# Optimization experiments

Measured on AMD Instinct MI355X. Metric: run time of the kernel, lower is better.

## Reference

```python
import jax, jax.numpy as jnp
import numpy as np

B, T, D = 8, 8192, 768
H, HD = 12, 64            # heads, head_dim
Q_STRIDE = 4              # flattened 2x2 q pooling
WINDOW = 64               # flattened mask-unit size after pooling
SCALE = HD ** -0.5


def setup_inputs() -> dict:
    key = jax.random.key(0)
    ks = jax.random.split(key, 5)
    return {
        "embeddings": jax.random.normal(ks[0], (B, T, D), jnp.float32),
        "qkv_w": jax.random.normal(ks[1], (3 * D, D), jnp.float32) * 0.02,
        "qkv_b": jax.random.normal(ks[2], (3 * D,), jnp.float32) * 0.02,
        "proj_w": jax.random.normal(ks[3], (D, D), jnp.float32) * 0.02,
        "proj_b": jax.random.normal(ks[4], (D,), jnp.float32) * 0.02,
    }


def reference(embeddings, qkv_w, qkv_b, proj_w, proj_b):
    b, t, _ = embeddings.shape
    nw = t // (Q_STRIDE * WINDOW)          # number of mask-unit windows
    seq = t // nw                           # tokens per window (pre q-pool)
    # qkv: [b, t, 3D] -> [b, seq, nw, 3, H, HD] (windows are interleaved along tokens)
    qkv = (embeddings @ qkv_w.T + qkv_b).reshape(b, seq, nw, 3, H, HD)
    qkv = jnp.transpose(qkv, (3, 0, 4, 2, 1, 5))  # [3, b, H, nw, seq, HD]
    q, k, v = qkv[0], qkv[1], qkv[2]
    # q max-pool over stride groups (interleaved split of seq)
    q = q.reshape(b, H, nw, Q_STRIDE, seq // Q_STRIDE, HD).max(axis=3)
    attn = jax.nn.softmax(
        jnp.einsum("bhwqd,bhwkd->bhwqk", q * SCALE, k), axis=-1
    )  # [b, H, nw, q_len, seq]
    out = jnp.einsum("bhwqk,bhwkd->bhwqd", attn, v)  # [b, H, nw, q_len, HD]
    out = jnp.transpose(out, (0, 3, 2, 1, 4)).reshape(b, -1, H * HD)
    out = out @ proj_w.T + proj_b
    return out, attn
```

## Files before the change

kernel.cpp:

```cpp
#include <hip/hip_runtime.h>
#include <hip/hip_bf16.h>


typedef float  f32x4  __attribute__((ext_vector_type(4)));
typedef __bf16 bf16x8 __attribute__((ext_vector_type(8)));

__device__ __forceinline__ unsigned short f2bf(float f) {
  unsigned int u = __float_as_uint(f);
  u += 0x7fffu + ((u >> 16) & 1u);
  return (unsigned short)(u >> 16);
}
__device__ __forceinline__ float bf2f(unsigned short b) {
  return __uint_as_float(((unsigned int)b) << 16);
}

#define GLOAD_LDS16(gptr, lptr) __builtin_amdgcn_global_load_lds( \
    (const __attribute__((address_space(1))) void*)(gptr),        \
    (__attribute__((address_space(3))) void*)(lptr), 16, 0, 0)

__global__ void cvt_bf16(const float* __restrict__ src,
                         unsigned short* __restrict__ dst, int n4) {
  int i = blockIdx.x * blockDim.x + threadIdx.x;
  const int stride = gridDim.x * blockDim.x;
  for (; i < n4; i += stride) {
    const float4 v = ((const float4*)src)[i];
    ushort4 o;
    o.x = f2bf(v.x); o.y = f2bf(v.y); o.z = f2bf(v.z); o.w = f2bf(v.w);
    ((ushort4*)dst)[i] = o;
  }
}

__global__ void cvt_w2(const float* __restrict__ s1, unsigned short* __restrict__ d1,
                       int n1_4,
                       const float* __restrict__ s2, unsigned short* __restrict__ d2,
                       int n2_4) {
  int i = blockIdx.x * blockDim.x + threadIdx.x;
  const int stride = gridDim.x * blockDim.x;
  const int tot = n1_4 + n2_4;
  for (; i < tot; i += stride) {
    const float4 v = (i < n1_4) ? ((const float4*)s1)[i]
                                : ((const float4*)s2)[i - n1_4];
    ushort4 o;
    o.x = f2bf(v.x); o.y = f2bf(v.y); o.z = f2bf(v.z); o.w = f2bf(v.w);
    if (i < n1_4) ((ushort4*)d1)[i] = o;
    else          ((ushort4*)d2)[i - n1_4] = o;
  }
}

template <int OUT_BF16>
__global__ __launch_bounds__(512, 2) void gemm256p(
    const unsigned short* __restrict__ A, const unsigned short* __restrict__ B,
    const float* __restrict__ bias, void* __restrict__ Cout,
    int M, int N, int K) {
  extern __shared__ char lds[];

  const int tid  = threadIdx.x;
  const int lane = tid & 63;
  const int wid  = tid >> 6;
  const int g16  = (lane >> 4) & 3;
  const int l15  = lane & 15;
  const int wm   = wid >> 2;
  const int wn   = wid & 3;

  const size_t bm = (size_t)blockIdx.x << 8;
  const int NT = K >> 6;
  const int NB = N >> 8;
  const int TT = NB * NT;

  const int srow = tid >> 2;
  const int csel = (((tid & 3) ^ ((tid >> 3) & 3)) << 3);
  const int ldst = wid * 1024;
  const unsigned short* pA0 = A + (bm + srow) * (size_t)K + csel;
  const unsigned short* pA1 = pA0 + (size_t)128 * K;
  const unsigned short* pB0 = B + (size_t)srow * K + csel;
  const unsigned short* pB1 = pB0 + (size_t)128 * K;

#define STAGE_A(koff, regbase)                                          \
  do {                                                                  \
    GLOAD_LDS16(pA0 + (koff), lds + (regbase) + ldst);                  \
    GLOAD_LDS16(pA1 + (koff), lds + (regbase) + 8192 + ldst);           \
  } while (0)
#define STAGE_B(boff, regbase)                                          \
  do {                                                                  \
    GLOAD_LDS16(pB0 + (boff), lds + (regbase) + ldst);                  \
    GLOAD_LDS16(pB1 + (boff), lds + (regbase) + 8192 + ldst);           \
  } while (0)

  const int s16  = ((g16 ^ ((l15 >> 1) & 3)) << 4);
  const int offA = (wm * 128 + l15) * 64 + s16;
  const int offB = (wn * 64 + l15) * 64 + s16;

  f32x4 acc[8][4];
  const f32x4 zero4 = {0.f, 0.f, 0.f, 0.f};
#pragma unroll
  for (int i = 0; i < 8; ++i)
#pragma unroll
    for (int j = 0; j < 4; ++j) acc[i][j] = zero4;

#define READ_A(par, kk, rh)                                              \
  { const char* rb = lds + (par) * 32768 + (kk) * 16384 + offA + (rh) * 4096; \
    af[0] = *(const bf16x8*)(rb);                                        \
    af[1] = *(const bf16x8*)(rb + 1024);                                 \
    af[2] = *(const bf16x8*)(rb + 2048);                                 \
    af[3] = *(const bf16x8*)(rb + 3072); }
#define READ_B(par, kk)                                                  \
  { const char* rb = lds + 65536 + (par) * 32768 + (kk) * 16384 + offB;  \
    bfv[0] = *(const bf16x8*)(rb);                                       \
    bfv[1] = *(const bf16x8*)(rb + 1024);                                \
    bfv[2] = *(const bf16x8*)(rb + 2048);                                \
    bfv[3] = *(const bf16x8*)(rb + 3072); }
#define MFMA16(rh)                                                       \
  _Pragma("unroll") for (int q = 0; q < 4; ++q)                          \
  _Pragma("unroll") for (int c = 0; c < 4; ++c)                          \
    acc[(rh) * 4 + q][c] = __builtin_amdgcn_mfma_f32_16x16x32_bf16(      \
        af[q], bfv[c], acc[(rh) * 4 + q][c], 0, 0, 0);
#define BAR() __builtin_amdgcn_s_barrier()
#define VMCNT8() asm volatile("s_waitcnt vmcnt(8)" ::: "memory")

  int    kk  = 0;
  int    bnC = 0;
  int    k1  = 64;
  int    k2  = 128;
  size_t rB1 = 0;
  size_t rB2 = 0;

  STAGE_A(0, 0);
  STAGE_B(0, 65536);
  STAGE_A(32, 16384);
  STAGE_B(32, 65536 + 16384);
  STAGE_A(64, 32768);
  STAGE_B(64, 65536 + 32768);
  VMCNT8();
  BAR();

  for (int s = 0; s < TT; ++s) {
    const int par  = s & 1;
    const int parn = par ^ 1;
    bf16x8 af[4], bfv[4];

    READ_A(par, 0, 0); READ_B(par, 0);
    STAGE_A(k1 + 32, parn * 32768 + 16384);
    BAR();
    __builtin_amdgcn_s_setprio(1); MFMA16(0); __builtin_amdgcn_s_setprio(0);
    BAR();

    READ_A(par, 0, 1);
    STAGE_B(rB1 + k1 + 32, 65536 + parn * 32768 + 16384);
    VMCNT8();
    BAR();
    __builtin_amdgcn_s_setprio(1); MFMA16(1); __builtin_amdgcn_s_setprio(0);
    BAR();

    READ_A(par, 1, 0); READ_B(par, 1);
    STAGE_A(k2, par * 32768);
    BAR();
    __builtin_amdgcn_s_setprio(1); MFMA16(0); __builtin_amdgcn_s_setprio(0);
    BAR();

    READ_A(par, 1, 1);
    STAGE_B(rB2 + k2, 65536 + par * 32768);
    VMCNT8();
    BAR();
    __builtin_amdgcn_s_setprio(1); MFMA16(1); __builtin_amdgcn_s_setprio(0);
    BAR();

    if (kk == NT - 1) {
#pragma unroll
      for (int ai = 0; ai < 8; ++ai) {
        const size_t row0 =
            bm + wm * 128 + (ai >> 2) * 64 + (ai & 3) * 16 + g16 * 4;
#pragma unroll
        for (int c = 0; c < 4; ++c) {
          const int col = bnC + wn * 64 + c * 16 + l15;
          const float bv = bias[col];
#pragma unroll
          for (int r = 0; r < 4; ++r) {
            const float v = acc[ai][c][r] + bv;
            const size_t idx = (row0 + r) * (size_t)N + col;
            if (OUT_BF16) ((unsigned short*)Cout)[idx] = f2bf(v);
            else          ((float*)Cout)[idx] = v;
          }
          acc[ai][c] = zero4;
        }
      }
      bnC += 256;
      kk = 0;
    } else {
      ++kk;
    }

    k1 = k2; rB1 = rB2;
    if (s + 3 < TT) {
      k2 += 64;
      if (k2 == K) { k2 = 0; rB2 += (size_t)256 * K; }
    }
  }
#undef STAGE_A
#undef STAGE_B
#undef READ_A
#undef READ_B
#undef MFMA16
#undef BAR
#undef VMCNT8
}

template <int OUT_BF16>
__global__ __launch_bounds__(512, 2) void gemm256t(
    const unsigned short* __restrict__ A, const unsigned short* __restrict__ B,
    const float* __restrict__ bias, void* __restrict__ Cout,
    int M, int N, int K) {
  extern __shared__ char lds[];

  const int tid  = threadIdx.x;
  const int lane = tid & 63;
  const int wid  = tid >> 6;
  const int g16  = (lane >> 4) & 3;
  const int l15  = lane & 15;
  const int wm   = wid >> 2;
  const int wn   = wid & 3;

  const int nbn = N >> 8;
  const int wg  = (blockIdx.x & 7) * ((int)gridDim.x >> 3) + (blockIdx.x >> 3);
  const size_t bm = (size_t)(wg / nbn) << 8;
  const size_t bn = (size_t)(wg % nbn) << 8;

  const int NT = K >> 6;

  const int srow = tid >> 2;
  const int csel = (((tid & 3) ^ ((tid >> 3) & 3)) << 3);
  const int ldst = wid * 1024;
  const unsigned short* pA0 = A + (bm + srow) * (size_t)K + csel;
  const unsigned short* pA1 = pA0 + (size_t)128 * K;
  const unsigned short* pB0 = B + (bn + srow) * (size_t)K + csel;
  const unsigned short* pB1 = pB0 + (size_t)128 * K;

#define STAGE(p0, p1, kcol, regbase)                                   \
  do {                                                                 \
    GLOAD_LDS16((p0) + (kcol), lds + (regbase) + ldst);                \
    GLOAD_LDS16((p1) + (kcol), lds + (regbase) + 8192 + ldst);         \
  } while (0)

  const int s16  = ((g16 ^ ((l15 >> 1) & 3)) << 4);
  const int offA = (wm * 128 + l15) * 64 + s16;
  const int offB = (wn * 64 + l15) * 64 + s16;

  f32x4 acc[8][4];
  const f32x4 zero4 = {0.f, 0.f, 0.f, 0.f};
#pragma unroll
  for (int i = 0; i < 8; ++i)
#pragma unroll
    for (int j = 0; j < 4; ++j) acc[i][j] = zero4;

#define READ_A(par, kk, rh)                                              \
  { const char* rb = lds + (par) * 32768 + (kk) * 16384 + offA + (rh) * 4096; \
    af[0] = *(const bf16x8*)(rb);                                        \
    af[1] = *(const bf16x8*)(rb + 1024);                                 \
    af[2] = *(const bf16x8*)(rb + 2048);                                 \
    af[3] = *(const bf16x8*)(rb + 3072); }
#define READ_B(par, kk)                                                  \
  { const char* rb = lds + 65536 + (par) * 32768 + (kk) * 16384 + offB;  \
    bfv[0] = *(const bf16x8*)(rb);                                       \
    bfv[1] = *(const bf16x8*)(rb + 1024);                                \
    bfv[2] = *(const bf16x8*)(rb + 2048);                                \
    bfv[3] = *(const bf16x8*)(rb + 3072); }
#define MFMA16(rh)                                                       \
  _Pragma("unroll") for (int q = 0; q < 4; ++q)                          \
  _Pragma("unroll") for (int c = 0; c < 4; ++c)                          \
    acc[(rh) * 4 + q][c] = __builtin_amdgcn_mfma_f32_16x16x32_bf16(      \
        af[q], bfv[c], acc[(rh) * 4 + q][c], 0, 0, 0);
#define BAR() __builtin_amdgcn_s_barrier()
#define VMCNT8() asm volatile("s_waitcnt vmcnt(8)" ::: "memory")

  STAGE(pA0, pA1, 0, 0);
  STAGE(pB0, pB1, 0, 65536);
  STAGE(pA0, pA1, 32, 16384);
  STAGE(pB0, pB1, 32, 65536 + 16384);
  {
    const int k1 = (NT > 1 ? 64 : 0);
    STAGE(pA0, pA1, k1, 32768);
    STAGE(pB0, pB1, k1, 65536 + 32768);
  }
  VMCNT8();
  BAR();

  for (int t = 0; t < NT; ++t) {
    const int par  = t & 1;
    const int parn = par ^ 1;
    const int kc1  = (t + 1 < NT ? t + 1 : NT - 1) * 64;
    const int kc2  = (t + 2 < NT ? t + 2 : NT - 1) * 64;
    bf16x8 af[4], bfv[4];

    READ_A(par, 0, 0); READ_B(par, 0);
    STAGE(pA0, pA1, kc1 + 32, parn * 32768 + 16384);
    BAR();
    __builtin_amdgcn_s_setprio(1); MFMA16(0); __builtin_amdgcn_s_setprio(0);
    BAR();

    READ_A(par, 0, 1);
    STAGE(pB0, pB1, kc1 + 32, 65536 + parn * 32768 + 16384);
    VMCNT8();
    BAR();
    __builtin_amdgcn_s_setprio(1); MFMA16(1); __builtin_amdgcn_s_setprio(0);
    BAR();

    READ_A(par, 1, 0); READ_B(par, 1);
    STAGE(pA0, pA1, kc2, par * 32768);
    BAR();
    __builtin_amdgcn_s_setprio(1); MFMA16(0); __builtin_amdgcn_s_setprio(0);
    BAR();

    READ_A(par, 1, 1);
    STAGE(pB0, pB1, kc2, 65536 + par * 32768);
    VMCNT8();
    BAR();
    __builtin_amdgcn_s_setprio(1); MFMA16(1); __builtin_amdgcn_s_setprio(0);
    BAR();
  }

#pragma unroll
  for (int ai = 0; ai < 8; ++ai) {
    const size_t row0 = bm + wm * 128 + (ai >> 2) * 64 + (ai & 3) * 16 + g16 * 4;
#pragma unroll
    for (int c = 0; c < 4; ++c) {
      const size_t col = bn + wn * 64 + c * 16 + l15;
      const float bv = bias[col];
#pragma unroll
      for (int r = 0; r < 4; ++r) {
        const float v = acc[ai][c][r] + bv;
        const size_t idx = (row0 + r) * N + col;
        if (OUT_BF16) ((unsigned short*)Cout)[idx] = f2bf(v);
        else          ((float*)Cout)[idx] = v;
      }
    }
  }
#undef STAGE
#undef READ_A
#undef READ_B
#undef MFMA16
#undef BAR
#undef VMCNT8
}

__global__ __launch_bounds__(256) void attn_kernel(
    const unsigned short* __restrict__ qkv,
    float* __restrict__ attn_out,
    unsigned short* __restrict__ Xws) {
  __shared__ unsigned short smem[32768];
  char* KP = (char*)smem;
  char* VT = (char*)(smem + 16384);

  const int tid  = threadIdx.x;
  const int lane = tid & 63;
  const int wid  = tid >> 6;
  const int g16  = lane >> 4;
  const int l15  = lane & 15;

  const int bid = blockIdx.x;
  const int w = bid & 31;
  const int h = (bid >> 5) % 12;
  const int b = bid / 384;

  const int s0 = tid >> 3;
  const int part = tid & 7;

#pragma unroll
  for (int p = 0; p < 8; ++p) {
    const int s = s0 + p * 32;
    const size_t gbase =
        ((size_t)b * 8192 + (size_t)s * 32 + w) * 2304 + h * 64 + part * 8;
    int4 kv = *(const int4*)(qkv + gbase + 768);
    *(int4*)(KP + ((s * 128 + part * 16) ^ ((s & 7) << 4))) = kv;
  }

#pragma unroll
  for (int p = 0; p < 2; ++p) {
    const int s = s0 * 4 + p * 128;
    const size_t gb0 =
        ((size_t)b * 8192 + (size_t)s * 32 + w) * 2304 + 1536 + h * 64 + part * 8;
    int4 x0 = *(const int4*)(qkv + gb0);
    int4 x1 = *(const int4*)(qkv + gb0 + 73728);
    int4 x2 = *(const int4*)(qkv + gb0 + 147456);
    int4 x3 = *(const int4*)(qkv + gb0 + 221184);
    const unsigned int* u0 = (const unsigned int*)&x0;
    const unsigned int* u1 = (const unsigned int*)&x1;
    const unsigned int* u2 = (const unsigned int*)&x2;
    const unsigned int* u3 = (const unsigned int*)&x3;
#pragma unroll
    for (int k = 0; k < 4; ++k) {
      const unsigned int lo01 = (u0[k] & 0xffffu) | (u1[k] << 16);
      const unsigned int lo23 = (u2[k] & 0xffffu) | (u3[k] << 16);
      const unsigned int hi01 = (u0[k] >> 16) | (u1[k] & 0xffff0000u);
      const unsigned int hi23 = (u2[k] >> 16) | (u3[k] & 0xffff0000u);
      const int dlo = part * 8 + 2 * k;
      const int dhi = dlo + 1;
      uint2 vlo; vlo.x = lo01; vlo.y = lo23;
      uint2 vhi; vhi.x = hi01; vhi.y = hi23;
      *(uint2*)(VT + ((dlo * 512 + s * 2) ^ ((dlo & 7) << 4))) = vlo;
      *(uint2*)(VT + ((dhi * 512 + s * 2) ^ ((dhi & 7) << 4))) = vhi;
    }
  }

  union BU { unsigned short u[8]; bf16x8 v; };
  BU aq0, aq1;
  {
    const int qrow = wid * 16 + l15;
    float q0[8], q1[8];
#pragma unroll
    for (int j = 0; j < 8; ++j) { q0[j] = -1e30f; q1[j] = -1e30f; }
#pragma unroll
    for (int g = 0; g < 4; ++g) {
      const size_t gbase =
          ((size_t)b * 8192 + (size_t)(g * 64 + qrow) * 32 + w) * 2304 +
          h * 64 + g16 * 8;
      int4 a = *(const int4*)(qkv + gbase);
      int4 c = *(const int4*)(qkv + gbase + 32);
      const unsigned short* pa = (const unsigned short*)&a;
      const unsigned short* pc = (const unsigned short*)&c;
#pragma unroll
      for (int j = 0; j < 8; ++j) {
        q0[j] = fmaxf(q0[j], bf2f(pa[j]));
        q1[j] = fmaxf(q1[j], bf2f(pc[j]));
      }
    }
#pragma unroll
    for (int j = 0; j < 8; ++j) {
      aq0.u[j] = (unsigned short)(__float_as_uint(q0[j]) >> 16);
      aq1.u[j] = (unsigned short)(__float_as_uint(q1[j]) >> 16);
    }
  }

  __syncthreads();

  f32x4 sacc[16];
  const f32x4 zero4 = {0.f, 0.f, 0.f, 0.f};
#pragma unroll
  for (int t = 0; t < 16; ++t) sacc[t] = zero4;
#pragma unroll
  for (int t = 0; t < 16; ++t) {
    const int srow = t * 16 + l15;
    bf16x8 bk0 = *(const bf16x8*)(KP + ((srow * 128 + 0  + g16 * 16) ^ ((srow & 7) << 4)));
    bf16x8 bk1 = *(const bf16x8*)(KP + ((srow * 128 + 64 + g16 * 16) ^ ((srow & 7) << 4)));
    sacc[t] = __builtin_amdgcn_mfma_f32_16x16x32_bf16(aq0.v, bk0, sacc[t], 0, 0, 0);
    sacc[t] = __builtin_amdgcn_mfma_f32_16x16x32_bf16(aq1.v, bk1, sacc[t], 0, 0, 0);
  }

  float inv_[4];
#pragma unroll
  for (int r = 0; r < 4; ++r) {
    float m = -1e30f;
#pragma unroll
    for (int t = 0; t < 16; ++t) { sacc[t][r] *= 0.125f; m = fmaxf(m, sacc[t][r]); }
#pragma unroll
    for (int off = 1; off < 16; off <<= 1) m = fmaxf(m, __shfl_xor(m, off, 64));
    float ssum = 0.f;
#pragma unroll
    for (int t = 0; t < 16; ++t) {
      float e = expf(sacc[t][r] - m);
      sacc[t][r] = e;
      ssum += e;
    }
#pragma unroll
    for (int off = 1; off < 16; off <<= 1) ssum += __shfl_xor(ssum, off, 64);
    inv_[r] = 1.f / ssum;
  }

  {
    float* ab = attn_out + ((size_t)bid * 64 + wid * 16) * 256;
#pragma unroll
    for (int t = 0; t < 16; ++t)
#pragma unroll
      for (int r = 0; r < 4; ++r) {
        const float p = sacc[t][r] * inv_[r];
        sacc[t][r] = p;
        ab[(size_t)(g16 * 4 + r) * 256 + t * 16 + l15] = p;
      }
  }

  __syncthreads();

  {
    char* PW = KP + wid * 8192;
#pragma unroll
    for (int t = 0; t < 16; ++t)
#pragma unroll
      for (int r = 0; r < 4; ++r) {
        const int row = g16 * 4 + r;
        *(unsigned short*)(PW + ((row * 512 + (t * 16 + l15) * 2) ^ ((row & 7) << 4))) =
            f2bf(sacc[t][r]);
      }
  }

  f32x4 oacc[4];
#pragma unroll
  for (int n = 0; n < 4; ++n) oacc[n] = zero4;
  {
    const char* PR = KP + wid * 8192;
#pragma unroll
    for (int kc = 0; kc < 8; ++kc) {
      bf16x8 pa = *(const bf16x8*)(PR + ((l15 * 512 + kc * 64 + g16 * 16) ^ ((l15 & 7) << 4)));
#pragma unroll
      for (int n = 0; n < 4; ++n) {
        const int d = n * 16 + l15;
        bf16x8 vv = *(const bf16x8*)(VT + ((d * 512 + kc * 64 + g16 * 16) ^ ((d & 7) << 4)));
        oacc[n] = __builtin_amdgcn_mfma_f32_16x16x32_bf16(pa, vv, oacc[n], 0, 0, 0);
      }
    }
  }

#pragma unroll
  for (int n = 0; n < 4; ++n)
#pragma unroll
    for (int r = 0; r < 4; ++r) {
      const int qi = wid * 16 + g16 * 4 + r;
      Xws[((size_t)b * 2048 + qi * 32 + w) * 768 + h * 64 + n * 16 + l15] =
          f2bf(oacc[n][r]);
    }
}

extern "C" void kernel_launch(void* const* d_in, const int* in_sizes, int n_in,
                              void* d_out, int out_size, void* d_ws, size_t ws_size,
                              hipStream_t stream) {
  const float* emb    = (const float*)d_in[0];
  const float* qkv_w  = (const float*)d_in[1];
  const float* qkv_b  = (const float*)d_in[2];
  const float* proj_w = (const float*)d_in[3];
  const float* proj_b = (const float*)d_in[4];
  float* out = (float*)d_out;

  char* ws = (char*)d_ws;
  unsigned short* embB   = (unsigned short*)(ws);
  unsigned short* wqkvB  = (unsigned short*)(ws + 100663296);
  unsigned short* wprojB = (unsigned short*)(ws + 104202240);
  unsigned short* qkvB   = (unsigned short*)(ws + 105381888);
  unsigned short* Xws    = (unsigned short*)(ws + 407371776);

  cvt_bf16<<<4096, 256, 0, stream>>>(emb, embB, 50331648 / 4);
  cvt_w2<<<2048, 256, 0, stream>>>(qkv_w, wqkvB, 1769472 / 4,
                                   proj_w, wprojB, 589824 / 4);

  hipFuncSetAttribute(reinterpret_cast<const void*>(&gemm256p<1>),
                      hipFuncAttributeMaxDynamicSharedMemorySize, 131072);
  gemm256p<1><<<256, 512, 131072, stream>>>(embB, wqkvB, qkv_b, qkvB,
                                            65536, 2304, 768);

  attn_kernel<<<3072, 256, 0, stream>>>(qkvB, out + 12582912, Xws);

  hipFuncSetAttribute(reinterpret_cast<const void*>(&gemm256t<0>),
                      hipFuncAttributeMaxDynamicSharedMemorySize, 131072);
  gemm256t<0><<<192, 512, 131072, stream>>>(Xws, wprojB, proj_b, out,
                                            16384, 768, 768);
}
```

Measured before the change: 464.7 us.

## Fuse fp32-to-bf16 activation conversion into QKV GEMM A-tile load path

Removes the standalone fp32-to-bf16 conversion pass over the embeddings. The QKV GEMM now stages fp32 A tiles into LDS and converts them to bf16 in registers with packed convert instructions before the MFMAs. The GEMM also changes from persistent 256-row blocks that loop over N to a 2D grid of 128x256 tiles with a grouped block-index swizzle. This saves a full read and write of the activations, but each tile loads twice as many bytes per A element and adds conversion ALU work inside the main loop.

Result: slower. 574.5 us (+23.6%).

```diff
diff --git a/kernel.cpp b/kernel.cpp
--- a/kernel.cpp
+++ b/kernel.cpp
@@ -17,18 +17,6 @@
 #define GLOAD_LDS16(gptr, lptr) __builtin_amdgcn_global_load_lds( \
     (const __attribute__((address_space(1))) void*)(gptr),        \
     (__attribute__((address_space(3))) void*)(lptr), 16, 0, 0)
-
-__global__ void cvt_bf16(const float* __restrict__ src,
-                         unsigned short* __restrict__ dst, int n4) {
-  int i = blockIdx.x * blockDim.x + threadIdx.x;
-  const int stride = gridDim.x * blockDim.x;
-  for (; i < n4; i += stride) {
-    const float4 v = ((const float4*)src)[i];
-    ushort4 o;
-    o.x = f2bf(v.x); o.y = f2bf(v.y); o.z = f2bf(v.z); o.w = f2bf(v.w);
-    ((ushort4*)dst)[i] = o;
-  }
-}
 
 __global__ void cvt_w2(const float* __restrict__ s1, unsigned short* __restrict__ d1,
                        int n1_4,
@@ -48,8 +36,8 @@
 }
 
 template <int OUT_BF16>
-__global__ __launch_bounds__(512, 2) void gemm256p(
-    const unsigned short* __restrict__ A, const unsigned short* __restrict__ B,
+__global__ __launch_bounds__(512, 2) void gemmf32a(
+    const float* __restrict__ A, const unsigned short* __restrict__ B,
     const float* __restrict__ bias, void* __restrict__ Cout,
     int M, int N, int K) {
   extern __shared__ char lds[];
@@ -62,28 +50,171 @@
   const int wm   = wid >> 2;
   const int wn   = wid & 3;
 
-  const size_t bm = (size_t)blockIdx.x << 8;
+  const int nbn = N >> 8;
+  const int wg  = (blockIdx.x & 7) * ((int)gridDim.x >> 3) + (blockIdx.x >> 3);
+  const size_t bm = (size_t)(wg / nbn) << 7;
+  const size_t bn = (size_t)(wg % nbn) << 8;
+
   const int NT = K >> 6;
-  const int NB = N >> 8;
-  const int TT = NB * NT;
+
+  const int rowA = wid * 16 + (lane >> 3);
+  const int slA  = lane & 7;
+  const float* pA0 = A + (bm + rowA) * (size_t)K + ((slA ^ (rowA & 7)) << 2);
+  const float* pA1 = pA0 + (size_t)8 * K;
+  const int rowB = wid * 32 + (lane >> 2);
+  const int slB  = lane & 3;
+  const unsigned short* pB0 = B + (bn + rowB) * (size_t)K + ((slB ^ (rowB & 3)) << 3);
+  const unsigned short* pB1 = pB0 + (size_t)16 * K;
+  const int dW = wid * 2048;
+
+#define STAGE_A(koff, regbase)                                          \
+  do {                                                                  \
+    GLOAD_LDS16(pA0 + (koff), lds + (regbase) + dW);                    \
+    GLOAD_LDS16(pA1 + (koff), lds + (regbase) + dW + 1024);             \
+  } while (0)
+#define STAGE_B(boff, regbase)                                          \
+  do {                                                                  \
+    GLOAD_LDS16(pB0 + (boff), lds + (regbase) + dW);                    \
+    GLOAD_LDS16(pB1 + (boff), lds + (regbase) + dW + 1024);             \
+  } while (0)
+
+  const int sA0    = ((2 * g16) ^ (l15 & 7)) << 4;
+  const int sA1    = ((2 * g16 + 1) ^ (l15 & 7)) << 4;
+  const int baseAr = (wm * 64 + l15) * 128;
+  const int sBr    = (g16 ^ (l15 & 3)) << 4;
+  const int baseBr = (wn * 64 + l15) * 64;
+
+  f32x4 acc[4][4];
+  const f32x4 zero4 = {0.f, 0.f, 0.f, 0.f};
+#pragma unroll
+  for (int i = 0; i < 4; ++i)
+#pragma unroll
+    for (int j = 0; j < 4; ++j) acc[i][j] = zero4;
+
+  f32x4 alo[4], ahi[4];
+  bf16x8 af[4], bfv[4];
+  union QU { int4 i; bf16x8 v; };
+
+#define READ_A(par, kh)                                                   \
+  { const char* ra = lds + (par) * 32768 + (kh) * 16384 + baseAr;         \
+    _Pragma("unroll") for (int m = 0; m < 4; ++m) {                       \
+      alo[m] = *(const f32x4*)(ra + m * 2048 + sA0);                      \
+      ahi[m] = *(const f32x4*)(ra + m * 2048 + sA1);                      \
+    } }
+#define CVT_A()                                                           \
+  { _Pragma("unroll") for (int m = 0; m < 4; ++m) {                       \
+      QU q;                                                               \
+      asm("v_cvt_pk_bf16_f32 %0, %1, %2" : "=v"(q.i.x) : "v"(alo[m][0]), "v"(alo[m][1])); \
+      asm("v_cvt_pk_bf16_f32 %0, %1, %2" : "=v"(q.i.y) : "v"(alo[m][2]), "v"(alo[m][3])); \
+      asm("v_cvt_pk_bf16_f32 %0, %1, %2" : "=v"(q.i.z) : "v"(ahi[m][0]), "v"(ahi[m][1])); \
+      asm("v_cvt_pk_bf16_f32 %0, %1, %2" : "=v"(q.i.w) : "v"(ahi[m][2]), "v"(ahi[m][3])); \
+      af[m] = q.v;                                                        \
+    } }
+#define READ_B(par, kh)                                                   \
+  { const char* rb = lds + 65536 + (par) * 32768 + (kh) * 16384 + baseBr + sBr; \
+    bfv[0] = *(const bf16x8*)(rb);                                        \
+    bfv[1] = *(const bf16x8*)(rb + 1024);                                 \
+    bfv[2] = *(const bf16x8*)(rb + 2048);                                 \
+    bfv[3] = *(const bf16x8*)(rb + 3072); }
+#define MFMA16()                                                          \
+  _Pragma("unroll") for (int m = 0; m < 4; ++m)                           \
+  _Pragma("unroll") for (int n = 0; n < 4; ++n)                           \
+    acc[m][n] = __builtin_amdgcn_mfma_f32_16x16x32_bf16(                  \
+        af[m], bfv[n], acc[m][n], 0, 0, 0);
+#define BAR() __builtin_amdgcn_s_barrier()
+#define VMCNT8() asm volatile("s_waitcnt vmcnt(8)" ::: "memory")
+
+  STAGE_A(0, 0);              STAGE_B(0, 65536);
+  STAGE_A(32, 16384);         STAGE_B(32, 65536 + 16384);
+  STAGE_A(64, 32768);         STAGE_B(64, 65536 + 32768);
+  VMCNT8();
+  BAR();
+
+  for (int t = 0; t < NT; ++t) {
+    const int par  = t & 1;
+    const int parn = par ^ 1;
+    const int kc1  = (t + 1 < NT ? t + 1 : NT - 1) * 64;
+    const int kc2  = (t + 2 < NT ? t + 2 : NT - 1) * 64;
+
+    READ_A(par, 0); READ_B(par, 0);
+    STAGE_A(kc1 + 32, parn * 32768 + 16384);
+    STAGE_B(kc1 + 32, 65536 + parn * 32768 + 16384);
+    VMCNT8();
+    BAR();
+    CVT_A();
+    __builtin_amdgcn_s_setprio(1); MFMA16(); __builtin_amdgcn_s_setprio(0);
+    BAR();
+
+    READ_A(par, 1); READ_B(par, 1);
+    STAGE_A(kc2, par * 32768);
+    STAGE_B(kc2, 65536 + par * 32768);
+    VMCNT8();
+    BAR();
+    CVT_A();
+    __builtin_amdgcn_s_setprio(1); MFMA16(); __builtin_amdgcn_s_setprio(0);
+    BAR();
+  }
+
+#pragma unroll
+  for (int m = 0; m < 4; ++m) {
+    const size_t row0 = bm + wm * 64 + m * 16 + g16 * 4;
+#pragma unroll
+    for (int n = 0; n < 4; ++n) {
+      const size_t col = bn + wn * 64 + n * 16 + l15;
+      const float bv = bias[col];
+#pragma unroll
+      for (int r = 0; r < 4; ++r) {
+        const float v = acc[m][n][r] + bv;
+        const size_t idx = (row0 + r) * N + col;
+        if (OUT_BF16) ((unsigned short*)Cout)[idx] = f2bf(v);
+        else          ((float*)Cout)[idx] = v;
+      }
+    }
+  }
+#undef STAGE_A
+#undef STAGE_B
+#undef READ_A
+#undef CVT_A
+#undef READ_B
+#undef MFMA16
+#undef BAR
+#undef VMCNT8
+}
+
+template <int OUT_BF16>
+__global__ __launch_bounds__(512, 2) void gemm256t(
+    const unsigned short* __restrict__ A, const unsigned short* __restrict__ B,
+    const float* __restrict__ bias, void* __restrict__ Cout,
+    int M, int N, int K) {
+  extern __shared__ char lds[];
+
+  const int tid  = threadIdx.x;
+  const int lane = tid & 63;
+  const int wid  = tid >> 6;
+  const int g16  = (lane >> 4) & 3;
+  const int l15  = lane & 15;
+  const int wm   = wid >> 2;
+  const int wn   = wid & 3;
+
+  const int nbn = N >> 8;
+  const int wg  = (blockIdx.x & 7) * ((int)gridDim.x >> 3) + (blockIdx.x >> 3);
+  const size_t bm = (size_t)(wg / nbn) << 8;
+  const size_t bn = (size_t)(wg % nbn) << 8;
+
+  const int NT = K >> 6;
 
   const int srow = tid >> 2;
   const int csel = (((tid & 3) ^ ((tid >> 3) & 3)) << 3);
   const int ldst = wid * 1024;
   const unsigned short* pA0 = A + (bm + srow) * (size_t)K + csel;
   const unsigned short* pA1 = pA0 + (size_t)128 * K;
-  const unsigned short* pB0 = B + (size_t)srow * K + csel;
+  const unsigned short* pB0 = B + (bn + srow) * (size_t)K + csel;
   const unsigned short* pB1 = pB0 + (size_t)128 * K;
 
-#define STAGE_A(koff, regbase)                                          \
-  do {                                                                  \
-    GLOAD_LDS16(pA0 + (koff), lds + (regbase) + ldst);                  \
-    GLOAD_LDS16(pA1 + (koff), lds + (regbase) + 8192 + ldst);           \
-  } while (0)
-#define STAGE_B(boff, regbase)                                          \
-  do {                                                                  \
-    GLOAD_LDS16(pB0 + (boff), lds + (regbase) + ldst);                  \
-    GLOAD_LDS16(pB1 + (boff), lds + (regbase) + 8192 + ldst);           \
+#define STAGE(p0, p1, kcol, regbase)                                   \
+  do {                                                                 \
+    GLOAD_LDS16((p0) + (kcol), lds + (regbase) + ldst);                \
+    GLOAD_LDS16((p1) + (kcol), lds + (regbase) + 8192 + ldst);         \
   } while (0)
 
   const int s16  = ((g16 ^ ((l15 >> 1) & 3)) << 4);
@@ -117,160 +248,6 @@
 #define BAR() __builtin_amdgcn_s_barrier()
 #define VMCNT8() asm volatile("s_waitcnt vmcnt(8)" ::: "memory")
 
-  int    kk  = 0;
-  int    bnC = 0;
-  int    k1  = 64;
-  int    k2  = 128;
-  size_t rB1 = 0;
-  size_t rB2 = 0;
-
-  STAGE_A(0, 0);
-  STAGE_B(0, 65536);
-  STAGE_A(32, 16384);
-  STAGE_B(32, 65536 + 16384);
-  STAGE_A(64, 32768);
-  STAGE_B(64, 65536 + 32768);
-  VMCNT8();
-  BAR();
-
-  for (int s = 0; s < TT; ++s) {
-    const int par  = s & 1;
-    const int parn = par ^ 1;
-    bf16x8 af[4], bfv[4];
-
-    READ_A(par, 0, 0); READ_B(par, 0);
-    STAGE_A(k1 + 32, parn * 32768 + 16384);
-    BAR();
-    __builtin_amdgcn_s_setprio(1); MFMA16(0); __builtin_amdgcn_s_setprio(0);
-    BAR();
-
-    READ_A(par, 0, 1);
-    STAGE_B(rB1 + k1 + 32, 65536 + parn * 32768 + 16384);
-    VMCNT8();
-    BAR();
-    __builtin_amdgcn_s_setprio(1); MFMA16(1); __builtin_amdgcn_s_setprio(0);
-    BAR();
-
-    READ_A(par, 1, 0); READ_B(par, 1);
-    STAGE_A(k2, par * 32768);
-    BAR();
-    __builtin_amdgcn_s_setprio(1); MFMA16(0); __builtin_amdgcn_s_setprio(0);
-    BAR();
-
-    READ_A(par, 1, 1);
-    STAGE_B(rB2 + k2, 65536 + par * 32768);
-    VMCNT8();
-    BAR();
-    __builtin_amdgcn_s_setprio(1); MFMA16(1); __builtin_amdgcn_s_setprio(0);
-    BAR();
-
-    if (kk == NT - 1) {
-#pragma unroll
-      for (int ai = 0; ai < 8; ++ai) {
-        const size_t row0 =
-            bm + wm * 128 + (ai >> 2) * 64 + (ai & 3) * 16 + g16 * 4;
-#pragma unroll
-        for (int c = 0; c < 4; ++c) {
-          const int col = bnC + wn * 64 + c * 16 + l15;
-          const float bv = bias[col];
-#pragma unroll
-          for (int r = 0; r < 4; ++r) {
-            const float v = acc[ai][c][r] + bv;
-            const size_t idx = (row0 + r) * (size_t)N + col;
-            if (OUT_BF16) ((unsigned short*)Cout)[idx] = f2bf(v);
-            else          ((float*)Cout)[idx] = v;
-          }
-          acc[ai][c] = zero4;
-        }
-      }
-      bnC += 256;
-      kk = 0;
-    } else {
-      ++kk;
-    }
-
-    k1 = k2; rB1 = rB2;
-    if (s + 3 < TT) {
-      k2 += 64;
-      if (k2 == K) { k2 = 0; rB2 += (size_t)256 * K; }
-    }
-  }
-#undef STAGE_A
-#undef STAGE_B
-#undef READ_A
-#undef READ_B
-#undef MFMA16
-#undef BAR
-#undef VMCNT8
-}
-
-template <int OUT_BF16>
-__global__ __launch_bounds__(512, 2) void gemm256t(
-    const unsigned short* __restrict__ A, const unsigned short* __restrict__ B,
-    const float* __restrict__ bias, void* __restrict__ Cout,
-    int M, int N, int K) {
-  extern __shared__ char lds[];
-
-  const int tid  = threadIdx.x;
-  const int lane = tid & 63;
-  const int wid  = tid >> 6;
-  const int g16  = (lane >> 4) & 3;
-  const int l15  = lane & 15;
-  const int wm   = wid >> 2;
-  const int wn   = wid & 3;
-
-  const int nbn = N >> 8;
-  const int wg  = (blockIdx.x & 7) * ((int)gridDim.x >> 3) + (blockIdx.x >> 3);
-  const size_t bm = (size_t)(wg / nbn) << 8;
-  const size_t bn = (size_t)(wg % nbn) << 8;
-
-  const int NT = K >> 6;
-
-  const int srow = tid >> 2;
-  const int csel = (((tid & 3) ^ ((tid >> 3) & 3)) << 3);
-  const int ldst = wid * 1024;
-  const unsigned short* pA0 = A + (bm + srow) * (size_t)K + csel;
-  const unsigned short* pA1 = pA0 + (size_t)128 * K;
-  const unsigned short* pB0 = B + (bn + srow) * (size_t)K + csel;
-  const unsigned short* pB1 = pB0 + (size_t)128 * K;
-
-#define STAGE(p0, p1, kcol, regbase)                                   \
-  do {                                                                 \
-    GLOAD_LDS16((p0) + (kcol), lds + (regbase) + ldst);                \
-    GLOAD_LDS16((p1) + (kcol), lds + (regbase) + 8192 + ldst);         \
-  } while (0)
-
-  const int s16  = ((g16 ^ ((l15 >> 1) & 3)) << 4);
-  const int offA = (wm * 128 + l15) * 64 + s16;
-  const int offB = (wn * 64 + l15) * 64 + s16;
-
-  f32x4 acc[8][4];
-  const f32x4 zero4 = {0.f, 0.f, 0.f, 0.f};
-#pragma unroll
-  for (int i = 0; i < 8; ++i)
-#pragma unroll
-    for (int j = 0; j < 4; ++j) acc[i][j] = zero4;
-
-#define READ_A(par, kk, rh)                                              \
-  { const char* rb = lds + (par) * 32768 + (kk) * 16384 + offA + (rh) * 4096; \
-    af[0] = *(const bf16x8*)(rb);                                        \
-    af[1] = *(const bf16x8*)(rb + 1024);                                 \
-    af[2] = *(const bf16x8*)(rb + 2048);                                 \
-    af[3] = *(const bf16x8*)(rb + 3072); }
-#define READ_B(par, kk)                                                  \
-  { const char* rb = lds + 65536 + (par) * 32768 + (kk) * 16384 + offB;  \
-    bfv[0] = *(const bf16x8*)(rb);                                       \
-    bfv[1] = *(const bf16x8*)(rb + 1024);                                \
-    bfv[2] = *(const bf16x8*)(rb + 2048);                                \
-    bfv[3] = *(const bf16x8*)(rb + 3072); }
-#define MFMA16(rh)                                                       \
-  _Pragma("unroll") for (int q = 0; q < 4; ++q)                          \
-  _Pragma("unroll") for (int c = 0; c < 4; ++c)                          \
-    acc[(rh) * 4 + q][c] = __builtin_amdgcn_mfma_f32_16x16x32_bf16(      \
-        af[q], bfv[c], acc[(rh) * 4 + q][c], 0, 0, 0);
-#define BAR() __builtin_amdgcn_s_barrier()
-#define VMCNT8() asm volatile("s_waitcnt vmcnt(8)" ::: "memory")
-
   STAGE(pA0, pA1, 0, 0);
   STAGE(pB0, pB1, 0, 65536);
   STAGE(pA0, pA1, 32, 16384);
@@ -528,20 +505,18 @@
   float* out = (float*)d_out;
 
   char* ws = (char*)d_ws;
-  unsigned short* embB   = (unsigned short*)(ws);
   unsigned short* wqkvB  = (unsigned short*)(ws + 100663296);
   unsigned short* wprojB = (unsigned short*)(ws + 104202240);
   unsigned short* qkvB   = (unsigned short*)(ws + 105381888);
   unsigned short* Xws    = (unsigned short*)(ws + 407371776);
 
-  cvt_bf16<<<4096, 256, 0, stream>>>(emb, embB, 50331648 / 4);
   cvt_w2<<<2048, 256, 0, stream>>>(qkv_w, wqkvB, 1769472 / 4,
                                    proj_w, wprojB, 589824 / 4);
 
-  hipFuncSetAttribute(reinterpret_cast<const void*>(&gemm256p<1>),
+  hipFuncSetAttribute(reinterpret_cast<const void*>(&gemmf32a<1>),
                       hipFuncAttributeMaxDynamicSharedMemorySize, 131072);
-  gemm256p<1><<<256, 512, 131072, stream>>>(embB, wqkvB, qkv_b, qkvB,
-                                            65536, 2304, 768);
+  gemmf32a<1><<<4608, 512, 131072, stream>>>(emb, wqkvB, qkv_b, qkvB,
+                                             65536, 2304, 768);
 
   attn_kernel<<<3072, 256, 0, stream>>>(qkvB, out + 12582912, Xws);
 
```
